# Optimization experiments

Measured on AMD Instinct MI355X. Metric: run time of the kernel, lower is better.

The kernel has to match this reference:

```python
import jax, jax.numpy as jnp
import numpy as np

NUM_HEADS = 16


def setup_inputs() -> dict:
    key = jax.random.key(0)
    k1, k2, k3, k4 = jax.random.split(key, 4)
    B, S, D = 4, 2048, 1024
    x = jax.random.normal(k1, (B, S, D), dtype=jnp.float32)
    mask = jnp.ones((B, S, S), dtype=jnp.int32)
    wq = jax.random.normal(k2, (D, D), dtype=jnp.float32) * (D ** -0.5)
    wk = jax.random.normal(k3, (D, D), dtype=jnp.float32) * (D ** -0.5)
    wv = jax.random.normal(k4, (D, D), dtype=jnp.float32) * (D ** -0.5)
    return {"x": x, "mask": mask, "wq": wq, "wk": wk, "wv": wv}


def reference(x, mask, wq, wk, wv):
    B, S, D = x.shape
    H = NUM_HEADS
    d_k = D // H
    # torch Linear (no bias): y = x @ W.T ; split heads -> [B,H,S,d_k]
    q = (x @ wq.T).reshape(B, S, H, d_k).transpose(0, 2, 1, 3)
    k = (x @ wk.T).reshape(B, S, H, d_k).transpose(0, 2, 1, 3)
    v = (x @ wv.T).reshape(B, S, H, d_k).transpose(0, 2, 1, 3)
    scale = 1.0 / np.sqrt(d_k).astype(np.float32)
    scores = jnp.einsum("bhqd,bhkd->bhqk", q, k) * scale  # [B,H,S,S]
    # masked_fill(mask==0, -1e9); mask broadcast over heads; NO softmax
    scores = jnp.where(mask[:, None, :, :] == 0, jnp.float32(-1e9), scores)
    # dropout is identity in eval mode
    attn = jnp.einsum("bhqk,bhkd->bhqd", scores, v)  # [B,H,S,d_k]
    return attn.transpose(0, 2, 1, 3).reshape(B, S, D)
```

## Files before the change

kernel.cpp:

```cpp
#include <hip/hip_runtime.h>
#include <hip/hip_bf16.h>


using u16 = unsigned short;
typedef __attribute__((ext_vector_type(8))) short  short8;
typedef __attribute__((ext_vector_type(4))) short  s16x4;
typedef __attribute__((ext_vector_type(4))) float  f32x4;
typedef __attribute__((ext_vector_type(4))) unsigned short u16x4;
typedef __attribute__((ext_vector_type(4))) int    i32x4;

#define DEV static __device__ __forceinline__

DEV u16 f2bh(float f) {
  __hip_bfloat16 h = __float2bfloat16(f);
  u16 r; __builtin_memcpy(&r, &h, 2); return r;
}

DEV int swz(int row, int col) { return (row << 6) + (col ^ ((row & 7) << 3)); }

template <typename T>
DEV void gload_lds16(const T* g, T* l) {
  __builtin_amdgcn_global_load_lds((const __attribute__((address_space(1))) unsigned int*)g,
                                   (__attribute__((address_space(3))) unsigned int*)l, 16, 0, 0);
}

__global__ __launch_bounds__(256) void k_prep(const float* __restrict__ x,
                                              const float* __restrict__ wq,
                                              const float* __restrict__ wk,
                                              const float* __restrict__ wv,
                                              const int* __restrict__ mask,
                                              u16* __restrict__ xb, u16* __restrict__ wb,
                                              int* __restrict__ flags) {
  const int t = threadIdx.x;
  if (blockIdx.x < 2048) {
    const int NX4 = 2097152;
    const int NW4 = 262144;
    const int total = NX4 + 3 * NW4;
    for (int i = blockIdx.x * 256 + t; i < total; i += 2048 * 256) {
      const float4* src; u16* dst; int j;
      if (i < NX4) { src = (const float4*)x; dst = xb; j = i; }
      else {
        int tw = i - NX4; int wsel = tw >> 18; j = tw & (NW4 - 1);
        src = (const float4*)(wsel == 0 ? wq : (wsel == 1 ? wk : wv));
        dst = wb + (size_t)wsel * 1048576;
      }
      float4 v = src[j];
      u16x4 o; o[0] = f2bh(v.x); o[1] = f2bh(v.y); o[2] = f2bh(v.z); o[3] = f2bh(v.w);
      *(u16x4*)(dst + (size_t)j * 4) = o;
    }
  } else {
    const int bx = blockIdx.x - 2048;
    const int b_ = bx >> 9, rem = bx & 511, qt = rem >> 5, kt = rem & 31;
    const size_t base = ((size_t)(b_ * 2048 + qt * 128)) * 2048 + kt * 64;
    int az = 0;
#pragma unroll
    for (int kk = 0; kk < 8; ++kk) {
      int i = t + kk * 256;
      int row = i >> 4, c4 = i & 15;
      i32x4 v = *(const i32x4*)(mask + base + (size_t)row * 2048 + c4 * 4);
      az |= (v.x == 0) | (v.y == 0) | (v.z == 0) | (v.w == 0);
    }
    __shared__ int red[4];
    unsigned long long bal = __ballot(az != 0);
    if ((t & 63) == 0) red[t >> 6] = (bal != 0ull);
    __syncthreads();
    if (t == 0) flags[bx] = red[0] | red[1] | red[2] | red[3];
  }
}

__global__ __launch_bounds__(256, 2) void k_proj(const u16* __restrict__ xb, const u16* __restrict__ wb,
                                                 u16* __restrict__ qb, u16* __restrict__ kb,
                                                 u16* __restrict__ vtb) {
  __shared__ u16 lA[128 * 64];
  __shared__ u16 lB[128 * 64];
  const int t = threadIdx.x, wid = t >> 6, lid = t & 63, ln = lid & 15, hi = lid >> 4;
  const int id = blockIdx.x;
  const int mt = (id & 7) + 8 * (id >> 6), nt = (id >> 3) & 7, which = blockIdx.y;
  const u16* wsrc = wb + (size_t)which * (1024 * 1024);
  const int wm = wid >> 1, wn = wid & 1;

  f32x4 acc[4][4];
#pragma unroll
  for (int a = 0; a < 4; ++a)
#pragma unroll
    for (int b2 = 0; b2 < 4; ++b2) acc[a][b2] = (f32x4){0.f, 0.f, 0.f, 0.f};

  for (int kt = 0; kt < 16; ++kt) {
    __syncthreads();
#pragma unroll
    for (int i = 0; i < 4; ++i) {
      int e = (i * 256 + t) * 8, row = e >> 6;
      int c = (e & 63) ^ ((row & 7) << 3);
      gload_lds16(xb + (size_t)(mt * 128 + row) * 1024 + kt * 64 + c, &lA[i * 2048 + wid * 512]);
      gload_lds16(wsrc + (size_t)(nt * 128 + row) * 1024 + kt * 64 + c, &lB[i * 2048 + wid * 512]);
    }
    __syncthreads();
#pragma unroll
    for (int ks = 0; ks < 2; ++ks) {
      short8 af[4], bfr[4];
#pragma unroll
      for (int mi = 0; mi < 4; ++mi) af[mi] = *(const short8*)&lA[swz(wm * 64 + mi * 16 + ln, ks * 32 + hi * 8)];
#pragma unroll
      for (int ni = 0; ni < 4; ++ni) bfr[ni] = *(const short8*)&lB[swz(wn * 64 + ni * 16 + ln, ks * 32 + hi * 8)];
#pragma unroll
      for (int mi = 0; mi < 4; ++mi)
#pragma unroll
        for (int ni = 0; ni < 4; ++ni)
          acc[mi][ni] = __builtin_amdgcn_mfma_f32_16x16x32_bf16(af[mi], bfr[ni], acc[mi][ni], 0, 0, 0);
    }
  }

  const int m0 = mt * 128 + wm * 64, n0 = nt * 128 + wn * 64;
  if (which == 2) {
#pragma unroll
    for (int mi = 0; mi < 4; ++mi)
#pragma unroll
      for (int ni = 0; ni < 4; ++ni) {
        int nn = n0 + ni * 16 + ln;
        int bb = m0 >> 11, sw = m0 & 2047, hh = nn >> 6, dd = nn & 63;
        u16x4 pk;
#pragma unroll
        for (int r = 0; r < 4; ++r) pk[r] = f2bh(acc[mi][ni][r]);
        *(u16x4*)(vtb + ((size_t)((bb * 16 + hh) * 64 + dd)) * 2048 + sw + hi * 16 + mi * 4) = pk;
      }
  } else {
    u16* dst = (which == 1) ? kb : qb;
    const float sc = (which == 0) ? 0.125f : 1.0f;
#pragma unroll
    for (int mi = 0; mi < 4; ++mi)
#pragma unroll
      for (int ni = 0; ni < 4; ++ni) {
        int nn = n0 + ni * 16 + ln;
        int hh = nn >> 6, dd = nn & 63;
#pragma unroll
        for (int r = 0; r < 4; ++r) {
          int m = m0 + mi * 16 + hi * 4 + r;
          int bb = m >> 11, ss = m & 2047;
          dst[((size_t)(bb * 16 + hh) * 2048 + ss) * 64 + dd] = f2bh(acc[mi][ni][r] * sc);
        }
      }
  }
}

__global__ __launch_bounds__(256, 4) void k_attn(const u16* __restrict__ qb, const u16* __restrict__ kb,
                                                 const u16* __restrict__ vtb, const int* __restrict__ mask,
                                                 const int* __restrict__ flags, float* __restrict__ out) {
  __shared__ __align__(16) u16 lds[16384];
  const int t = threadIdx.x, wid = t >> 6, lid = t & 63, ln = lid & 15, hi = lid >> 4;
  const int id = blockIdx.x;
  const int qt = (id >> 3) & 15, bh = (id & 7) + 8 * (id >> 7);
  const int b_ = bh >> 4, h = bh & 15;
  const u16* Qg = qb + (size_t)bh * (2048 * 64);
  const u16* Kg = kb + (size_t)bh * (2048 * 64);
  const u16* Vg = vtb + (size_t)bh * (64 * 2048);
  const int* flagp = flags + (b_ * 16 + qt) * 32;
  const int* maskp = mask + (size_t)b_ * (2048 * 2048);

  short8 aq[2][2];
#pragma unroll
  for (int mi = 0; mi < 2; ++mi)
#pragma unroll
    for (int ks = 0; ks < 2; ++ks)
      aq[mi][ks] = *(const short8*)(Qg + (size_t)(qt * 128 + wid * 32 + mi * 16 + ln) * 64 + ks * 32 + hi * 8);

#pragma unroll
  for (int i = 0; i < 2; ++i) {
    int e = (i * 256 + t) * 8, row = e >> 6;
    int c = (e & 63) ^ ((row & 7) << 3);
    gload_lds16(Kg + (size_t)row * 64 + c, &lds[i * 2048 + wid * 512]);
    gload_lds16(Vg + (size_t)row * 2048 + c, &lds[4096 + i * 2048 + wid * 512]);
  }
  __syncthreads();

  f32x4 ot[4][2];
#pragma unroll
  for (int di = 0; di < 4; ++di)
#pragma unroll
    for (int mi = 0; mi < 2; ++mi) ot[di][mi] = (f32x4){0.f, 0.f, 0.f, 0.f};

  int cur = 0;
  for (int kt = 0; kt < 32; ++kt) {
    if (kt + 1 < 32) {
#pragma unroll
      for (int i = 0; i < 2; ++i) {
        int e = (i * 256 + t) * 8, row = e >> 6;
        int c = (e & 63) ^ ((row & 7) << 3);
        gload_lds16(Kg + (size_t)((kt + 1) * 64 + row) * 64 + c, &lds[(cur ^ 1) * 8192 + i * 2048 + wid * 512]);
        gload_lds16(Vg + (size_t)row * 2048 + (kt + 1) * 64 + c, &lds[(cur ^ 1) * 8192 + 4096 + i * 2048 + wid * 512]);
      }
    }
    const u16* bK = lds + cur * 8192;
    const u16* bV = lds + cur * 8192 + 4096;

    f32x4 sa[4][2];
#pragma unroll
    for (int ni = 0; ni < 4; ++ni)
#pragma unroll
      for (int mi = 0; mi < 2; ++mi) sa[ni][mi] = (f32x4){0.f, 0.f, 0.f, 0.f};
    __builtin_amdgcn_s_setprio(1);
#pragma unroll
    for (int ks = 0; ks < 2; ++ks) {
      short8 bk[4];
#pragma unroll
      for (int ni = 0; ni < 4; ++ni) bk[ni] = *(const short8*)&bK[swz(ni * 16 + ln, ks * 32 + hi * 8)];
#pragma unroll
      for (int ni = 0; ni < 4; ++ni)
#pragma unroll
        for (int mi = 0; mi < 2; ++mi)
          sa[ni][mi] = __builtin_amdgcn_mfma_f32_16x16x32_bf16(bk[ni], aq[mi][ks], sa[ni][mi], 0, 0, 0);
    }
    __builtin_amdgcn_s_setprio(0);

    int flg = flagp[kt];
    s16x4 pt[4][2];
#pragma unroll
    for (int ni = 0; ni < 4; ++ni)
#pragma unroll
      for (int mi = 0; mi < 2; ++mi) {
#pragma unroll
        for (int r = 0; r < 4; ++r) {
          float p = sa[ni][mi][r];
          if (flg) {
            int qg = qt * 128 + wid * 32 + mi * 16 + ln;
            int kvg = kt * 64 + ni * 16 + hi * 4 + r;
            if (maskp[(size_t)qg * 2048 + kvg] == 0) p = -1e9f;
          }
          pt[ni][mi][r] = (short)f2bh(p);
        }
      }

    __builtin_amdgcn_s_setprio(1);
#pragma unroll
    for (int di = 0; di < 4; ++di) {
      short8 vv0 = *(const short8*)&bV[swz(di * 16 + ln, hi * 16)];
      short8 vv1 = *(const short8*)&bV[swz(di * 16 + ln, hi * 16 + 8)];
      s16x4 vt[4];
      vt[0] = __builtin_shufflevector(vv0, vv0, 0, 1, 2, 3);
      vt[1] = __builtin_shufflevector(vv0, vv0, 4, 5, 6, 7);
      vt[2] = __builtin_shufflevector(vv1, vv1, 0, 1, 2, 3);
      vt[3] = __builtin_shufflevector(vv1, vv1, 4, 5, 6, 7);
#pragma unroll
      for (int ni = 0; ni < 4; ++ni)
#pragma unroll
        for (int mi = 0; mi < 2; ++mi)
          ot[di][mi] = __builtin_amdgcn_mfma_f32_16x16x16bf16_1k(vt[ni], pt[ni][mi], ot[di][mi], 0, 0, 0);
    }
    __builtin_amdgcn_s_setprio(0);

    __syncthreads();
    cur ^= 1;
  }

  float* op = out + ((size_t)b_ * 2048 + qt * 128) * 1024 + h * 64;
#pragma unroll
  for (int di = 0; di < 4; ++di)
#pragma unroll
    for (int mi = 0; mi < 2; ++mi) {
      int q = wid * 32 + mi * 16 + ln;
      int d = di * 16 + hi * 4;
      *(f32x4*)(op + (size_t)q * 1024 + d) = ot[di][mi];
    }
}

extern "C" void kernel_launch(void* const* d_in, const int* in_sizes, int n_in,
                              void* d_out, int out_size, void* d_ws, size_t ws_size,
                              hipStream_t stream) {
  const float* x   = (const float*)d_in[0];
  const int*  mask = (const int*)d_in[1];
  const float* wq  = (const float*)d_in[2];
  const float* wk  = (const float*)d_in[3];
  const float* wv  = (const float*)d_in[4];
  float* out = (float*)d_out;

  char* ws = (char*)d_ws;
  const size_t XB_OFF = 0;
  const size_t WB_OFF = 16777216;
  const size_t QB_OFF = 23068672;
  const size_t KB_OFF = 39845888;
  const size_t VT_OFF = 56623104;
  const size_t FL_OFF = 73400320;
  if (ws_size < FL_OFF + 8192) return;

  u16* xb  = (u16*)(ws + XB_OFF);
  u16* wb  = (u16*)(ws + WB_OFF);
  u16* qb  = (u16*)(ws + QB_OFF);
  u16* kb  = (u16*)(ws + KB_OFF);
  u16* vtb = (u16*)(ws + VT_OFF);
  int* flags = (int*)(ws + FL_OFF);

  k_prep<<<4096, 256, 0, stream>>>(x, wq, wk, wv, mask, xb, wb, flags);
  k_proj<<<dim3(512, 3), 256, 0, stream>>>(xb, wb, qb, kb, vtb);
  k_attn<<<1024, 256, 0, stream>>>(qb, kb, vtb, mask, flags, out);
}
```

Measured before the change: 270.1 us.

## Use 16x16x32 MFMA for PV with packed bf16 convert and permlane swaps

Replaces the 16x16x16 bf16 MFMAs for scores×V with 16x16x32 MFMAs. The score fragments are converted with v_cvt_pk_bf16_f32 and rearranged across lanes with permlane32/16 swaps to fit the wider K operand. To match, the V-transpose store layout in the projection kernel changes to natural row order. Mask application is hoisted into a single flag-guarded pass, and k_proj's launch bounds rise to 3 blocks per CU. These changes aim to halve the MFMA instruction count and the per-element conversion cost, but depend on the lane permutation and the V layout agreeing exactly.

```diff
diff --git a/kernel.cpp b/kernel.cpp
--- a/kernel.cpp
+++ b/kernel.cpp
@@ -4,9 +4,9 @@
 
 using u16 = unsigned short;
 typedef __attribute__((ext_vector_type(8))) short  short8;
-typedef __attribute__((ext_vector_type(4))) short  s16x4;
 typedef __attribute__((ext_vector_type(4))) float  f32x4;
 typedef __attribute__((ext_vector_type(4))) unsigned short u16x4;
+typedef __attribute__((ext_vector_type(4))) unsigned int   u32x4;
 typedef __attribute__((ext_vector_type(4))) int    i32x4;
 
 #define DEV static __device__ __forceinline__
@@ -15,6 +15,14 @@
   __hip_bfloat16 h = __float2bfloat16(f);
   u16 r; __builtin_memcpy(&r, &h, 2); return r;
 }
+
+DEV unsigned cvtpk(float lo, float hi) {
+  unsigned r;
+  asm("v_cvt_pk_bf16_f32 %0, %1, %2" : "=v"(r) : "v"(lo), "v"(hi));
+  return r;
+}
+
+DEV short8 u2s8(u32x4 v) { short8 r; __builtin_memcpy(&r, &v, 16); return r; }
 
 DEV int swz(int row, int col) { return (row << 6) + (col ^ ((row & 7) << 3)); }
 
@@ -68,7 +76,7 @@
   }
 }
 
-__global__ __launch_bounds__(256, 2) void k_proj(const u16* __restrict__ xb, const u16* __restrict__ wb,
+__global__ __launch_bounds__(256, 3) void k_proj(const u16* __restrict__ xb, const u16* __restrict__ wb,
                                                  u16* __restrict__ qb, u16* __restrict__ kb,
                                                  u16* __restrict__ vtb) {
   __shared__ u16 lA[128 * 64];
@@ -116,12 +124,13 @@
     for (int mi = 0; mi < 4; ++mi)
 #pragma unroll
       for (int ni = 0; ni < 4; ++ni) {
+        int mm = m0 + mi * 16 + hi * 4;
         int nn = n0 + ni * 16 + ln;
-        int bb = m0 >> 11, sw = m0 & 2047, hh = nn >> 6, dd = nn & 63;
+        int bb = mm >> 11, s0 = mm & 2047, hh = nn >> 6, dd = nn & 63;
         u16x4 pk;
 #pragma unroll
         for (int r = 0; r < 4; ++r) pk[r] = f2bh(acc[mi][ni][r]);
-        *(u16x4*)(vtb + ((size_t)((bb * 16 + hh) * 64 + dd)) * 2048 + sw + hi * 16 + mi * 4) = pk;
+        *(u16x4*)(vtb + ((size_t)((bb * 16 + hh) * 64 + dd)) * 2048 + s0) = pk;
       }
   } else {
     u16* dst = (which == 1) ? kb : qb;
@@ -211,39 +220,45 @@
     }
     __builtin_amdgcn_s_setprio(0);
 
-    int flg = flagp[kt];
-    s16x4 pt[4][2];
-#pragma unroll
-    for (int ni = 0; ni < 4; ++ni)
-#pragma unroll
-      for (int mi = 0; mi < 2; ++mi) {
-#pragma unroll
-        for (int r = 0; r < 4; ++r) {
-          float p = sa[ni][mi][r];
-          if (flg) {
+    if (flagp[kt]) {
+#pragma unroll
+      for (int ni = 0; ni < 4; ++ni)
+#pragma unroll
+        for (int mi = 0; mi < 2; ++mi)
+#pragma unroll
+          for (int r = 0; r < 4; ++r) {
             int qg = qt * 128 + wid * 32 + mi * 16 + ln;
             int kvg = kt * 64 + ni * 16 + hi * 4 + r;
-            if (maskp[(size_t)qg * 2048 + kvg] == 0) p = -1e9f;
+            if (maskp[(size_t)qg * 2048 + kvg] == 0) sa[ni][mi][r] = -1e9f;
           }
-          pt[ni][mi][r] = (short)f2bh(p);
-        }
+    }
+
+    u32x4 pb[2][2];
+#pragma unroll
+    for (int nb = 0; nb < 2; ++nb)
+#pragma unroll
+      for (int mi = 0; mi < 2; ++mi) {
+        unsigned a0 = cvtpk(sa[2 * nb][mi][0], sa[2 * nb][mi][1]);
+        unsigned a1 = cvtpk(sa[2 * nb][mi][2], sa[2 * nb][mi][3]);
+        unsigned b0 = cvtpk(sa[2 * nb + 1][mi][0], sa[2 * nb + 1][mi][1]);
+        unsigned b1 = cvtpk(sa[2 * nb + 1][mi][2], sa[2 * nb + 1][mi][3]);
+        asm("v_permlane32_swap_b32 %0, %1" : "+v"(a0), "+v"(b0));
+        asm("v_permlane32_swap_b32 %0, %1" : "+v"(a1), "+v"(b1));
+        asm("v_permlane16_swap_b32 %0, %1" : "+v"(a0), "+v"(b0));
+        asm("v_permlane16_swap_b32 %0, %1" : "+v"(a1), "+v"(b1));
+        pb[nb][mi] = (u32x4){a0, a1, b0, b1};
       }
 
     __builtin_amdgcn_s_setprio(1);
 #pragma unroll
     for (int di = 0; di < 4; ++di) {
-      short8 vv0 = *(const short8*)&bV[swz(di * 16 + ln, hi * 16)];
-      short8 vv1 = *(const short8*)&bV[swz(di * 16 + ln, hi * 16 + 8)];
-      s16x4 vt[4];
-      vt[0] = __builtin_shufflevector(vv0, vv0, 0, 1, 2, 3);
-      vt[1] = __builtin_shufflevector(vv0, vv0, 4, 5, 6, 7);
-      vt[2] = __builtin_shufflevector(vv1, vv1, 0, 1, 2, 3);
-      vt[3] = __builtin_shufflevector(vv1, vv1, 4, 5, 6, 7);
-#pragma unroll
-      for (int ni = 0; ni < 4; ++ni)
-#pragma unroll
-        for (int mi = 0; mi < 2; ++mi)
-          ot[di][mi] = __builtin_amdgcn_mfma_f32_16x16x16bf16_1k(vt[ni], pt[ni][mi], ot[di][mi], 0, 0, 0);
+      short8 v0 = *(const short8*)&bV[swz(di * 16 + ln, hi * 8)];
+      short8 v1 = *(const short8*)&bV[swz(di * 16 + ln, 32 + hi * 8)];
+#pragma unroll
+      for (int mi = 0; mi < 2; ++mi) {
+        ot[di][mi] = __builtin_amdgcn_mfma_f32_16x16x32_bf16(v0, u2s8(pb[0][mi]), ot[di][mi], 0, 0, 0);
+        ot[di][mi] = __builtin_amdgcn_mfma_f32_16x16x32_bf16(v1, u2s8(pb[1][mi]), ot[di][mi], 0, 0, 0);
+      }
     }
     __builtin_amdgcn_s_setprio(0);
 
```

Measured after the change: 258.9 us. -4.1%, faster.
